# Performance work log

Measured on AMD Instinct MI355X. Metric: run time of the kernel, lower is better.

## Reference

```python
import jax, jax.numpy as jnp
import numpy as np

N_NODES = 100000
N_EDGES = 1600000
NFEAT, NHID, NCLASS = 512, 128, 64


def setup_inputs() -> dict:
    key = jax.random.key(0)
    ks = jax.random.split(key, 8)
    y = jax.random.normal(ks[0], (N_NODES, NFEAT), dtype=jnp.float32)
    src = jax.random.randint(ks[1], (N_EDGES,), 0, N_NODES, dtype=jnp.int64)
    dst = jax.random.randint(ks[2], (N_EDGES,), 0, N_NODES, dtype=jnp.int64)
    edge_w = jax.random.uniform(ks[3], (N_EDGES,), dtype=jnp.float32)
    # GraphConvolution params (Glorot-ish scale)
    W1 = jax.random.normal(ks[4], (NFEAT, NHID), dtype=jnp.float32) / np.sqrt(NFEAT)
    b1 = jax.random.normal(ks[5], (NHID,), dtype=jnp.float32) * 0.01
    W2 = jax.random.normal(ks[6], (NHID, NCLASS), dtype=jnp.float32) / np.sqrt(NHID)
    b2 = jax.random.normal(ks[7], (NCLASS,), dtype=jnp.float32) * 0.01
    return {"y": y, "src": src, "dst": dst, "edge_w": edge_w,
            "W1": W1, "b1": b1, "W2": W2, "b2": b2}


def _graph_conv(x, W, b, src, dst, edge_w, n_nodes):
    # support = x @ W ; out = spmm(adj, support) + b  (adj in COO form)
    support = x @ W                                   # [N, out_dim]
    msgs = support[src] * edge_w[:, None]             # [E, out_dim] gather
    agg = jax.ops.segment_sum(msgs, dst, num_segments=n_nodes)  # scatter-add
    return agg + b


def reference(y, src, dst, edge_w, W1, b1, W2, b2):
    h = jax.nn.leaky_relu(_graph_conv(y, W1, b1, src, dst, edge_w, N_NODES),
                          negative_slope=0.01)        # F.leaky_relu default
    y_embedding = h
    logits = _graph_conv(h, W2, b2, src, dst, edge_w, N_NODES)
    return (jax.nn.softmax(logits, axis=1), y_embedding)
```

## Files before the change

kernel.cpp:

```cpp
#include <hip/hip_runtime.h>
#include <hip/hip_fp16.h>

#define NN 100000
#define NE 1600000
#define F0 512
#define F1 128
#define F2 64

typedef short bf16x8 __attribute__((ext_vector_type(8)));
typedef float f32x4  __attribute__((ext_vector_type(4)));

static __device__ __forceinline__ unsigned short f2bf(float f) {
    unsigned int u = __float_as_uint(f);
    return (unsigned short)((u + 0x7FFFu + ((u >> 16) & 1u)) >> 16);
}

static __device__ __forceinline__ unsigned short f2h(float f) {
    __half h = __float2half(f);
    return *(unsigned short*)&h;
}

static __device__ __forceinline__ float2 h2f2(unsigned int u) {
    __half2 h = *(__half2*)&u;
    return __half22float2(h);
}

__global__ __launch_bounds__(256)
void wt_kernel(const float* __restrict__ W1, const float* __restrict__ W2,
               unsigned short* __restrict__ W1t, unsigned short* __restrict__ W2t)
{
    int i = blockIdx.x * 256 + threadIdx.x;
    if (i < F0 * F1) {
        int n = i / F0, k = i % F0;
        W1t[i] = f2bf(W1[k * F1 + n]);
    } else {
        int j = i - F0 * F1;
        if (j < F1 * F2) {
            int n = j / F1, k = j % F1;
            W2t[j] = f2bf(W2[k * F2 + n]);
        }
    }
}

template<int BM, int BN, int BK, int TN>
__global__ __launch_bounds__(256)
void mfma_gemm(const float* __restrict__ A, const unsigned short* __restrict__ Bt,
               unsigned short* __restrict__ C, int M, int K, int N)
{
    constexpr int LDA = BK + 8;
    constexpr int LDB = BK + 8;
    __shared__ unsigned short As[BM * LDA];
    __shared__ unsigned short Bs[BN * LDB];

    const int tid  = threadIdx.x;
    const int wave = tid >> 6;
    const int lane = tid & 63;
    const int lr   = lane & 15;
    const int quad = lane >> 4;
    const int row0 = blockIdx.x * BM;

    f32x4 acc[2][TN];
#pragma unroll
    for (int i = 0; i < 2; i++)
#pragma unroll
        for (int j = 0; j < TN; j++) acc[i][j] = (f32x4)0.f;

    for (int k0 = 0; k0 < K; k0 += BK) {
#pragma unroll
        for (int l = tid; l < BM * (BK / 4); l += 256) {
            int m  = l / (BK / 4);
            int kq = l % (BK / 4);
            int rg = row0 + m; if (rg >= M) rg = M - 1;
            float4 v = *(const float4*)(A + (long long)rg * K + k0 + kq * 4);
            ushort4 b = make_ushort4(f2bf(v.x), f2bf(v.y), f2bf(v.z), f2bf(v.w));
            *(ushort4*)(&As[m * LDA + kq * 4]) = b;
        }
#pragma unroll
        for (int l = tid; l < BN * (BK / 8); l += 256) {
            int n  = l / (BK / 8);
            int ko = l % (BK / 8);
            uint4 v = *(const uint4*)(Bt + (long long)n * K + k0 + ko * 8);
            *(uint4*)(&Bs[n * LDB + ko * 8]) = v;
        }
        __syncthreads();

#pragma unroll
        for (int kk = 0; kk < BK; kk += 32) {
            bf16x8 a[2], b[TN];
#pragma unroll
            for (int tm = 0; tm < 2; tm++)
                a[tm] = *(const bf16x8*)(&As[(wave * 32 + tm * 16 + lr) * LDA + kk + quad * 8]);
#pragma unroll
            for (int tn = 0; tn < TN; tn++)
                b[tn] = *(const bf16x8*)(&Bs[(tn * 16 + lr) * LDB + kk + quad * 8]);
#pragma unroll
            for (int tm = 0; tm < 2; tm++)
#pragma unroll
                for (int tn = 0; tn < TN; tn++)
                    acc[tm][tn] = __builtin_amdgcn_mfma_f32_16x16x32_bf16(
                        a[tm], b[tn], acc[tm][tn], 0, 0, 0);
        }
        __syncthreads();
    }

#pragma unroll
    for (int tm = 0; tm < 2; tm++) {
#pragma unroll
        for (int r = 0; r < 4; r++) {
            int row = row0 + wave * 32 + tm * 16 + quad * 4 + r;
            if (row < M) {
#pragma unroll
                for (int tn = 0; tn < TN; tn++)
                    C[(long long)row * N + tn * 16 + lr] = f2h(acc[tm][tn][r]);
            }
        }
    }
}

__global__ __launch_bounds__(256)
void hist_kernel(const int* __restrict__ dst, int* __restrict__ cnt,
                 int* __restrict__ rank, int ne)
{
    int e = blockIdx.x * 256 + threadIdx.x;
    if (e < ne) rank[e] = atomicAdd(&cnt[dst[e]], 1);
}

__global__ __launch_bounds__(256)
void scan1_kernel(const int* __restrict__ cnt, int* __restrict__ rowptr,
                  int* __restrict__ bsum, int n)
{
    __shared__ int s[256];
    int t = threadIdx.x;
    int i = blockIdx.x * 256 + t;
    int v = (i < n) ? cnt[i] : 0;
    s[t] = v;
    __syncthreads();
#pragma unroll
    for (int off = 1; off < 256; off <<= 1) {
        int x = (t >= off) ? s[t - off] : 0;
        __syncthreads();
        s[t] += x;
        __syncthreads();
    }
    if (i < n) rowptr[i] = s[t] - v;
    if (t == 255) bsum[blockIdx.x] = s[255];
}

__global__ __launch_bounds__(512)
void scan2_kernel(int* __restrict__ bsum, int nb, int* __restrict__ rowptr, int n, int ne)
{
    __shared__ int s[512];
    int t = threadIdx.x;
    int v = (t < nb) ? bsum[t] : 0;
    s[t] = v;
    __syncthreads();
#pragma unroll
    for (int off = 1; off < 512; off <<= 1) {
        int x = (t >= off) ? s[t - off] : 0;
        __syncthreads();
        s[t] += x;
        __syncthreads();
    }
    if (t < nb) bsum[t] = s[t] - v;
    if (t == 0) rowptr[n] = ne;
}

__global__ __launch_bounds__(256)
void scan3_kernel(int* __restrict__ rowptr, const int* __restrict__ bsum, int n)
{
    int i = blockIdx.x * 256 + threadIdx.x;
    if (i < n) rowptr[i] += bsum[i >> 8];
}

__global__ __launch_bounds__(256)
void fill_kernel(const int* __restrict__ src, const int* __restrict__ dst,
                 const float* __restrict__ ew, const int* __restrict__ rowptr,
                 const int* __restrict__ rank, int2* __restrict__ rec, int ne)
{
    int e = blockIdx.x * 256 + threadIdx.x;
    if (e >= ne) return;
    int d = dst[e];
    int pos = rowptr[d] + rank[e];
    rec[pos] = make_int2(src[e], __float_as_int(ew[e]));
}

__global__ __launch_bounds__(256)
void agg1_kernel(const unsigned int* __restrict__ sup, const int2* __restrict__ rec,
                 const int* __restrict__ rowptr, const float2* __restrict__ b1,
                 float2* __restrict__ h, int n)
{
    int node = blockIdx.x * 4 + (threadIdx.x >> 6);
    int lane = threadIdx.x & 63;
    if (node >= n) return;

    int j   = rowptr[node];
    int end = rowptr[node + 1];
    float2 acc = make_float2(0.f, 0.f);

    for (; j + 4 <= end; j += 4) {
        int2 r0 = rec[j];
        int2 r1 = rec[j + 1];
        int2 r2 = rec[j + 2];
        int2 r3 = rec[j + 3];
        unsigned int u0 = sup[(long long)r0.x * 64 + lane];
        unsigned int u1 = sup[(long long)r1.x * 64 + lane];
        unsigned int u2 = sup[(long long)r2.x * 64 + lane];
        unsigned int u3 = sup[(long long)r3.x * 64 + lane];
        float w0 = __int_as_float(r0.y);
        float w1 = __int_as_float(r1.y);
        float w2 = __int_as_float(r2.y);
        float w3 = __int_as_float(r3.y);
        float2 f0 = h2f2(u0);
        float2 f1 = h2f2(u1);
        float2 f2 = h2f2(u2);
        float2 f3 = h2f2(u3);
        acc.x = fmaf(f0.x, w0, acc.x);  acc.y = fmaf(f0.y, w0, acc.y);
        acc.x = fmaf(f1.x, w1, acc.x);  acc.y = fmaf(f1.y, w1, acc.y);
        acc.x = fmaf(f2.x, w2, acc.x);  acc.y = fmaf(f2.y, w2, acc.y);
        acc.x = fmaf(f3.x, w3, acc.x);  acc.y = fmaf(f3.y, w3, acc.y);
    }
    for (; j < end; j++) {
        int2 r0 = rec[j];
        unsigned int u0 = sup[(long long)r0.x * 64 + lane];
        float w0 = __int_as_float(r0.y);
        float2 f0 = h2f2(u0);
        acc.x = fmaf(f0.x, w0, acc.x);
        acc.y = fmaf(f0.y, w0, acc.y);
    }

    float2 bb = b1[lane];
    acc.x += bb.x;
    acc.y += bb.y;
    acc.x = acc.x > 0.f ? acc.x : 0.01f * acc.x;
    acc.y = acc.y > 0.f ? acc.y : 0.01f * acc.y;
    h[(long long)node * 64 + lane] = acc;
}

__global__ __launch_bounds__(256)
void agg2_kernel(const unsigned short* __restrict__ sup, const int2* __restrict__ rec,
                 const int* __restrict__ rowptr, const float* __restrict__ b2,
                 float* __restrict__ out, int n)
{
    int node = blockIdx.x * 4 + (threadIdx.x >> 6);
    int lane = threadIdx.x & 63;
    if (node >= n) return;

    int j   = rowptr[node];
    int end = rowptr[node + 1];
    float acc = 0.f;

    for (; j + 4 <= end; j += 4) {
        int2 r0 = rec[j];
        int2 r1 = rec[j + 1];
        int2 r2 = rec[j + 2];
        int2 r3 = rec[j + 3];
        unsigned short u0 = sup[(long long)r0.x * 64 + lane];
        unsigned short u1 = sup[(long long)r1.x * 64 + lane];
        unsigned short u2 = sup[(long long)r2.x * 64 + lane];
        unsigned short u3 = sup[(long long)r3.x * 64 + lane];
        acc = fmaf(__half2float(*(__half*)&u0), __int_as_float(r0.y), acc);
        acc = fmaf(__half2float(*(__half*)&u1), __int_as_float(r1.y), acc);
        acc = fmaf(__half2float(*(__half*)&u2), __int_as_float(r2.y), acc);
        acc = fmaf(__half2float(*(__half*)&u3), __int_as_float(r3.y), acc);
    }
    for (; j < end; j++) {
        int2 r0 = rec[j];
        unsigned short u0 = sup[(long long)r0.x * 64 + lane];
        acc = fmaf(__half2float(*(__half*)&u0), __int_as_float(r0.y), acc);
    }

    float v = acc + b2[lane];
    float m = v;
#pragma unroll
    for (int off = 32; off; off >>= 1) m = fmaxf(m, __shfl_xor(m, off, 64));
    float e = __expf(v - m);
    float s = e;
#pragma unroll
    for (int off = 32; off; off >>= 1) s += __shfl_xor(s, off, 64);
    out[(long long)node * 64 + lane] = e / s;
}

extern "C" void kernel_launch(void* const* d_in, const int* in_sizes, int n_in,
                              void* d_out, int out_size, void* d_ws, size_t ws_size,
                              hipStream_t stream)
{
    const float* y   = (const float*)d_in[0];
    const int*   src = (const int*)  d_in[1];
    const int*   dst = (const int*)  d_in[2];
    const float* ew  = (const float*)d_in[3];
    const float* W1  = (const float*)d_in[4];
    const float* b1  = (const float*)d_in[5];
    const float* W2  = (const float*)d_in[6];
    const float* b2  = (const float*)d_in[7];

    float* out     = (float*)d_out;
    float* softout = out;
    float* h       = out + (size_t)NN * F2;

    char* ws = (char*)d_ws;
    size_t o = 0;
    auto alloc = [&](size_t bytes) -> void* {
        void* p = ws + o;
        o = (o + bytes + 255) & ~(size_t)255;
        return p;
    };
    unsigned short* sup  = (unsigned short*)alloc((size_t)NN * F1 * 2);
    int2*           rec  = (int2*)          alloc((size_t)NE * 8);
    int*            rank = (int*)           alloc((size_t)NE * 4);
    int*            rowptr = (int*)         alloc((size_t)(NN + 2) * 4);
    int*            cnt  = (int*)           alloc((size_t)NN * 4);
    int*            bsum = (int*)           alloc(512 * 4);
    unsigned short* W1t  = (unsigned short*)alloc((size_t)F0 * F1 * 2);
    unsigned short* W2t  = (unsigned short*)alloc((size_t)F1 * F2 * 2);

    const int NB = (NN + 255) / 256;

    wt_kernel<<<(F0 * F1 + F1 * F2 + 255) / 256, 256, 0, stream>>>(W1, W2, W1t, W2t);

    hipMemsetAsync(cnt, 0, (size_t)NN * 4, stream);
    hist_kernel<<<(NE + 255) / 256, 256, 0, stream>>>(dst, cnt, rank, NE);
    scan1_kernel<<<NB, 256, 0, stream>>>(cnt, rowptr, bsum, NN);
    scan2_kernel<<<1, 512, 0, stream>>>(bsum, NB, rowptr, NN, NE);
    scan3_kernel<<<NB, 256, 0, stream>>>(rowptr, bsum, NN);
    fill_kernel<<<(NE + 255) / 256, 256, 0, stream>>>(src, dst, ew, rowptr, rank, rec, NE);

    mfma_gemm<128, 128, 64, 8>
        <<<(NN + 127) / 128, 256, 0, stream>>>(y, W1t, sup, NN, F0, F1);
    agg1_kernel<<<(NN + 3) / 4, 256, 0, stream>>>(
        (const unsigned int*)sup, rec, rowptr, (const float2*)b1, (float2*)h, NN);

    mfma_gemm<128, 64, 64, 4>
        <<<(NN + 127) / 128, 256, 0, stream>>>(h, W2t, sup, NN, F1, F2);
    agg2_kernel<<<(NN + 3) / 4, 256, 0, stream>>>(
        sup, rec, rowptr, b2, softout, NN);
}
```

Baseline: 616.9 us.

## Fuse layer-2 GEMM into first aggregation kernel via per-block MFMA

The first aggregation kernel now processes 16 nodes per block. It stages the leaky-ReLU outputs as bf16 in shared memory, then multiplies them by W2 with 16x16x32 bf16 MFMA instructions, writing the layer-2 support directly to a new buffer. This removes the separate second GEMM launch and its re-read of h from global memory. In exchange, each wave handles four nodes serially, which may reduce memory-level parallelism in the gather phase, and it adds a block-wide barrier before the MFMA step.

Result: no change. 612.7 us (-0.7%).

```diff
diff --git a/kernel.cpp b/kernel.cpp
--- a/kernel.cpp
+++ b/kernel.cpp
@@ -185,55 +185,86 @@
 }
 
 __global__ __launch_bounds__(256)
-void agg1_kernel(const unsigned int* __restrict__ sup, const int2* __restrict__ rec,
-                 const int* __restrict__ rowptr, const float2* __restrict__ b1,
-                 float2* __restrict__ h, int n)
-{
-    int node = blockIdx.x * 4 + (threadIdx.x >> 6);
-    int lane = threadIdx.x & 63;
-    if (node >= n) return;
-
-    int j   = rowptr[node];
-    int end = rowptr[node + 1];
-    float2 acc = make_float2(0.f, 0.f);
-
-    for (; j + 4 <= end; j += 4) {
-        int2 r0 = rec[j];
-        int2 r1 = rec[j + 1];
-        int2 r2 = rec[j + 2];
-        int2 r3 = rec[j + 3];
-        unsigned int u0 = sup[(long long)r0.x * 64 + lane];
-        unsigned int u1 = sup[(long long)r1.x * 64 + lane];
-        unsigned int u2 = sup[(long long)r2.x * 64 + lane];
-        unsigned int u3 = sup[(long long)r3.x * 64 + lane];
-        float w0 = __int_as_float(r0.y);
-        float w1 = __int_as_float(r1.y);
-        float w2 = __int_as_float(r2.y);
-        float w3 = __int_as_float(r3.y);
-        float2 f0 = h2f2(u0);
-        float2 f1 = h2f2(u1);
-        float2 f2 = h2f2(u2);
-        float2 f3 = h2f2(u3);
-        acc.x = fmaf(f0.x, w0, acc.x);  acc.y = fmaf(f0.y, w0, acc.y);
-        acc.x = fmaf(f1.x, w1, acc.x);  acc.y = fmaf(f1.y, w1, acc.y);
-        acc.x = fmaf(f2.x, w2, acc.x);  acc.y = fmaf(f2.y, w2, acc.y);
-        acc.x = fmaf(f3.x, w3, acc.x);  acc.y = fmaf(f3.y, w3, acc.y);
-    }
-    for (; j < end; j++) {
-        int2 r0 = rec[j];
-        unsigned int u0 = sup[(long long)r0.x * 64 + lane];
-        float w0 = __int_as_float(r0.y);
-        float2 f0 = h2f2(u0);
-        acc.x = fmaf(f0.x, w0, acc.x);
-        acc.y = fmaf(f0.y, w0, acc.y);
-    }
+void agg1_fused_kernel(const unsigned int* __restrict__ sup, const int2* __restrict__ rec,
+                       const int* __restrict__ rowptr, const float2* __restrict__ b1,
+                       const unsigned short* __restrict__ W2t,
+                       float2* __restrict__ h, unsigned short* __restrict__ sup2, int n)
+{
+    constexpr int LDH = F1 + 8;
+    __shared__ unsigned short hsb[16 * LDH];
+
+    const int tid  = threadIdx.x;
+    const int w    = tid >> 6;
+    const int lane = tid & 63;
+    const int base = blockIdx.x * 16;
 
     float2 bb = b1[lane];
-    acc.x += bb.x;
-    acc.y += bb.y;
-    acc.x = acc.x > 0.f ? acc.x : 0.01f * acc.x;
-    acc.y = acc.y > 0.f ? acc.y : 0.01f * acc.y;
-    h[(long long)node * 64 + lane] = acc;
+
+#pragma unroll
+    for (int i = 0; i < 4; i++) {
+        int row  = w * 4 + i;
+        int node = base + row;
+        float2 acc = make_float2(0.f, 0.f);
+        if (node < n) {
+            int j   = rowptr[node];
+            int end = rowptr[node + 1];
+            for (; j + 4 <= end; j += 4) {
+                int2 r0 = rec[j];
+                int2 r1 = rec[j + 1];
+                int2 r2 = rec[j + 2];
+                int2 r3 = rec[j + 3];
+                unsigned int u0 = sup[(long long)r0.x * 64 + lane];
+                unsigned int u1 = sup[(long long)r1.x * 64 + lane];
+                unsigned int u2 = sup[(long long)r2.x * 64 + lane];
+                unsigned int u3 = sup[(long long)r3.x * 64 + lane];
+                float w0 = __int_as_float(r0.y);
+                float w1 = __int_as_float(r1.y);
+                float w2 = __int_as_float(r2.y);
+                float w3 = __int_as_float(r3.y);
+                float2 f0 = h2f2(u0);
+                float2 f1 = h2f2(u1);
+                float2 f2 = h2f2(u2);
+                float2 f3 = h2f2(u3);
+                acc.x = fmaf(f0.x, w0, acc.x);  acc.y = fmaf(f0.y, w0, acc.y);
+                acc.x = fmaf(f1.x, w1, acc.x);  acc.y = fmaf(f1.y, w1, acc.y);
+                acc.x = fmaf(f2.x, w2, acc.x);  acc.y = fmaf(f2.y, w2, acc.y);
+                acc.x = fmaf(f3.x, w3, acc.x);  acc.y = fmaf(f3.y, w3, acc.y);
+            }
+            for (; j < end; j++) {
+                int2 r0 = rec[j];
+                unsigned int u0 = sup[(long long)r0.x * 64 + lane];
+                float w0 = __int_as_float(r0.y);
+                float2 f0 = h2f2(u0);
+                acc.x = fmaf(f0.x, w0, acc.x);
+                acc.y = fmaf(f0.y, w0, acc.y);
+            }
+            acc.x += bb.x;
+            acc.y += bb.y;
+            acc.x = acc.x > 0.f ? acc.x : 0.01f * acc.x;
+            acc.y = acc.y > 0.f ? acc.y : 0.01f * acc.y;
+            h[(long long)node * 64 + lane] = acc;
+        }
+        ushort2 hv = (node < n) ? make_ushort2(f2bf(acc.x), f2bf(acc.y))
+                                : make_ushort2(0, 0);
+        *(ushort2*)(&hsb[row * LDH + lane * 2]) = hv;
+    }
+    __syncthreads();
+
+    const int lr   = lane & 15;
+    const int quad = lane >> 4;
+    f32x4 acc2 = (f32x4)0.f;
+#pragma unroll
+    for (int kk = 0; kk < F1; kk += 32) {
+        bf16x8 a = *(const bf16x8*)(&hsb[lr * LDH + kk + quad * 8]);
+        bf16x8 b = *(const bf16x8*)(W2t + (w * 16 + lr) * F1 + kk + quad * 8);
+        acc2 = __builtin_amdgcn_mfma_f32_16x16x32_bf16(a, b, acc2, 0, 0, 0);
+    }
+#pragma unroll
+    for (int r = 0; r < 4; r++) {
+        int node = base + quad * 4 + r;
+        if (node < n)
+            sup2[(long long)node * 64 + w * 16 + lr] = f2h(acc2[r]);
+    }
 }
 
 __global__ __launch_bounds__(256)
@@ -305,6 +336,7 @@
         return p;
     };
     unsigned short* sup  = (unsigned short*)alloc((size_t)NN * F1 * 2);
+    unsigned short* sup2 = (unsigned short*)alloc((size_t)NN * F2 * 2);
     int2*           rec  = (int2*)          alloc((size_t)NE * 8);
     int*            rank = (int*)           alloc((size_t)NE * 4);
     int*            rowptr = (int*)         alloc((size_t)(NN + 2) * 4);
@@ -326,11 +358,11 @@
 
     mfma_gemm<128, 128, 64, 8>
         <<<(NN + 127) / 128, 256, 0, stream>>>(y, W1t, sup, NN, F0, F1);
-    agg1_kernel<<<(NN + 3) / 4, 256, 0, stream>>>(
-        (const unsigned int*)sup, rec, rowptr, (const float2*)b1, (float2*)h, NN);
-
-    mfma_gemm<128, 64, 64, 4>
-        <<<(NN + 127) / 128, 256, 0, stream>>>(h, W2t, sup, NN, F1, F2);
+
+    agg1_fused_kernel<<<(NN + 15) / 16, 256, 0, stream>>>(
+        (const unsigned int*)sup, rec, rowptr, (const float2*)b1, W2t,
+        (float2*)h, sup2, NN);
+
     agg2_kernel<<<(NN + 3) / 4, 256, 0, stream>>>(
-        sup, rec, rowptr, b2, softout, NN);
-}
+        sup2, rec, rowptr, b2, softout, NN);
+}
```
